# Performance work log

Hardware: AMD Instinct MI355X
Metric: run time of the kernel (lower is better)

## Reference

```python
import jax, jax.numpy as jnp
import numpy as np

H = 50      # hidden_size (fixed in source)
IN = 7      # input_size = len(features)
B = 1024    # batch
T = 512     # seq_len
FC1 = 25
OUT = 1


def setup_inputs() -> dict:
    key = jax.random.key(0)
    ks = jax.random.split(key, 24)
    s = 1.0 / np.sqrt(H)  # PyTorch LSTM/Linear default uniform init scale

    def u(k, shape):
        return jax.random.uniform(k, shape, jnp.float32, -s, s)

    d = {"x": jax.random.normal(ks[0], (B, T, IN), jnp.float32)}
    # 4 stacked LSTM layers total: lstm1 has 2 layers (in=7 then 50), lstm2 has 2 layers (in=50)
    in_sizes = [IN, H, H, H]
    for l, isz in enumerate(in_sizes):
        d[f"Wih{l}"] = u(ks[1 + 4 * l], (4 * H, isz))
        d[f"Whh{l}"] = u(ks[2 + 4 * l], (4 * H, H))
        d[f"bih{l}"] = u(ks[3 + 4 * l], (4 * H,))
        d[f"bhh{l}"] = u(ks[4 + 4 * l], (4 * H,))
    d["W1"] = u(ks[17], (FC1, H))
    d["b1"] = u(ks[18], (FC1,))
    d["W2"] = u(ks[19], (OUT, FC1))
    d["b2"] = u(ks[20], (OUT,))
    return d


def _lstm_layer(x, Wih, Whh, bih, bhh):
    # x: [B, T, in] -> hidden sequence [B, T, H]. PyTorch gate order: i, f, g, o.
    b, t, _ = x.shape
    h = Whh.shape[1]
    # Precompute input projection for all timesteps in one big GEMM: [T, B, 4H]
    xp = jnp.einsum('bti,gi->tbg', x, Wih) + (bih + bhh)

    def step(carry, xt):
        hs, cs = carry
        gates = xt + hs @ Whh.T                      # [B, 4H]
        i, f, g, o = jnp.split(gates, 4, axis=-1)
        i = jax.nn.sigmoid(i)
        f = jax.nn.sigmoid(f)
        g = jnp.tanh(g)
        o = jax.nn.sigmoid(o)
        cs = f * cs + i * g
        hs = o * jnp.tanh(cs)
        return (hs, cs), hs

    h0 = jnp.zeros((b, h), x.dtype)
    _, hseq = jax.lax.scan(step, (h0, h0), xp)       # hseq: [T, B, H]
    return hseq.transpose(1, 0, 2)


def reference(x, Wih0, Whh0, bih0, bhh0, Wih1, Whh1, bih1, bhh1,
              Wih2, Whh2, bih2, bhh2, Wih3, Whh3, bih3, bhh3,
              W1, b1, W2, b2):
    out = x
    layers = [(Wih0, Whh0, bih0, bhh0), (Wih1, Whh1, bih1, bhh1),
              (Wih2, Whh2, bih2, bhh2), (Wih3, Whh3, bih3, bhh3)]
    for Wih, Whh, bih, bhh in layers:
        out = _lstm_layer(out, Wih, Whh, bih, bhh)
    h = out[:, -1, :]                                # last timestep [B, H]
    # dropout is identity in eval mode
    h = jax.nn.relu(h @ W1.T + b1)
    return h @ W2.T + b2                             # [B, 1]
```

## Files before the change

### kernel.cpp

```cpp
#include <hip/hip_runtime.h>


#define H 50
#define INSZ 7
#define TT 512
#define NL 4
#define FC1N 25
#define BPG 4
#define NBLK 256
#define NTHREADS 1024
#define HS 80
#define RROW (BPG * HS)
#define BIASL 56

typedef _Float16 half_t;
typedef __attribute__((ext_vector_type(8))) _Float16 half8_t;
typedef __attribute__((ext_vector_type(4))) float float4_t;

struct Params {
  const float* x;
  const float* Wih[NL];
  const float* Whh[NL];
  const float* bih[NL];
  const float* bhh[NL];
  const float* W1;
  const float* b1;
  const float* W2;
  const float* b2;
  float* out;
};

#define MFMA16(A, B, C) __builtin_amdgcn_mfma_f32_16x16x32_f16((A), (B), (C), 0, 0, 0)
#define EXP2F(x) __builtin_amdgcn_exp2f(x)
#define RCPF(x) __builtin_amdgcn_rcpf(x)

__global__ __launch_bounds__(NTHREADS, 4) void lstm_r7(Params p) {
  __shared__ __align__(16) half_t Xring[64][BPG][HS];
  __shared__ __align__(16) half_t Hbuf[NL - 1][2][BPG][HS];
  __shared__ float fc_h[BPG][H];
  __shared__ float fc1_buf[BPG][FC1N];

  const int tid = threadIdx.x;
  const int b0 = blockIdx.x * BPG;
  const int lane = tid & 63;
  const int quad = lane >> 4;
  const int col = lane & 15;
  const int glay = tid >> 8;
  const int wl = (((tid >> 6) & 3) + glay) & 3;

  half8_t afrag[4][4];
#pragma unroll
  for (int t4 = 0; t4 < 4; ++t4) {
#pragma unroll
    for (int g = 0; g < 4; ++g) {
      half8_t v;
#pragma unroll
      for (int j = 0; j < 8; ++j) {
        const int r = wl * 64 + t4 * 16 + col;
        const int u = r >> 2, q = r & 3;
        const int k = g * 32 + quad * 8 + j;
        float wv = 0.0f;
        if (u < H) {
          const int row = q * H + u;
          if (glay == 0) {
            if (k < INSZ) wv = p.Wih[0][row * INSZ + k];
            else if (k == 7) wv = p.bih[0][row] + p.bhh[0][row];
            else if (k >= 8 && k < 8 + H) wv = p.Whh[0][row * H + (k - 8)];
          } else if (glay == 1) {
            if (k == 7) wv = p.bih[1][row] + p.bhh[1][row];
            else if (k >= 8 && k < 8 + H) wv = p.Wih[1][row * H + (k - 8)];
            else if (k >= 64 && k < 64 + H) wv = p.Whh[1][row * H + (k - 64)];
          } else {
            if (k < H) wv = p.Wih[glay][row * H + k];
            else if (k == BIASL) wv = p.bih[glay][row] + p.bhh[glay][row];
            else if (k >= 64 && k < 64 + H) wv = p.Whh[glay][row * H + (k - 64)];
          }
        }
        v[j] = (half_t)wv;
      }
      afrag[t4][g] = v;
    }
  }

  {
    unsigned* xz = (unsigned*)Xring;
    const int nx = 64 * BPG * HS / 2;
    for (int i = tid; i < nx; i += NTHREADS) xz[i] = 0u;
    unsigned* hz = (unsigned*)Hbuf;
    const int nh = (NL - 1) * 2 * BPG * HS / 2;
    for (int i = tid; i < nh; i += NTHREADS) hz[i] = 0u;
  }
  __syncthreads();
  for (int i = tid; i < 64 * BPG; i += NTHREADS)
    Xring[i >> 2][i & 3][7] = (half_t)1.0f;
  if (tid < (NL - 1) * 2 * BPG) {
    const int l = tid >> 3, pr = (tid >> 2) & 1, b = tid & 3;
    Hbuf[l][pr][b][BIASL] = (half_t)1.0f;
  }
  for (int i = tid; i < 64 * BPG * INSZ; i += NTHREADS) {
    const int t = i / (BPG * INSZ), rem = i % (BPG * INSZ);
    const int b = rem / INSZ, k = rem % INSZ;
    Xring[t][b][k] = (half_t)p.x[((size_t)(b0 + b) * TT + t) * INSZ + k];
  }
  __syncthreads();

  const int bb = col & 3;
  const int tsel = col >> 2;
  const int uu = 16 * wl + 4 * tsel + quad;
  const bool updact = (uu < H);

  const half_t* ring_rd0 = &Xring[0][bb][quad * 8];
  half_t* ring_st0 = &Xring[0][bb][8 + uu];

  const half_t* inb[2] = {nullptr, nullptr};
  const half_t* ownb[2] = {nullptr, nullptr};
  half_t* stb[2] = {nullptr, nullptr};
  if (glay >= 1) {
    ownb[0] = &Hbuf[glay - 1][0][bb][quad * 8];
    ownb[1] = &Hbuf[glay - 1][1][bb][quad * 8];
    stb[0] = &Hbuf[glay - 1][1][bb][uu];
    stb[1] = &Hbuf[glay - 1][0][bb][uu];
  }
  if (glay >= 2) {
    inb[0] = &Hbuf[glay - 2][1][bb][quad * 8];
    inb[1] = &Hbuf[glay - 2][0][bb][quad * 8];
  }
  const int pe = glay & 1, po = pe ^ 1;
  const half_t* in_e = inb[pe];
  const half_t* in_o = inb[po];
  const half_t* own_e = ownb[pe];
  const half_t* own_o = ownb[po];
  half_t* st_e = stb[pe];
  half_t* st_o = stb[po];

  const bool xwave = (glay == 0) && (wl == 3);
  const int rb = lane >> 5;
  const int rt = lane & 31;

  float cst = 0.0f;
  const float4_t fzc = {0.0f, 0.0f, 0.0f, 0.0f};

#define TICK_BODY(PIN, POWN, PST, FCW)                                          \
  {                                                                             \
    float4_t a0 = fzc, a1 = fzc, a2 = fzc, a3 = fzc;                            \
    if (glay == 0) {                                                            \
      const half8_t v0 = *(const half8_t*)(PIN);                                \
      const half8_t v1 = *(const half8_t*)((PIN) + 32);                         \
      if (wl != 3) {                                                            \
        a0 = MFMA16(afrag[0][0], v0, a0); a1 = MFMA16(afrag[1][0], v0, a1);     \
        a2 = MFMA16(afrag[2][0], v0, a2); a3 = MFMA16(afrag[3][0], v0, a3);     \
        a0 = MFMA16(afrag[0][1], v1, a0); a1 = MFMA16(afrag[1][1], v1, a1);     \
        a2 = MFMA16(afrag[2][1], v1, a2); a3 = MFMA16(afrag[3][1], v1, a3);     \
      } else {                                                                  \
        a0 = MFMA16(afrag[0][0], v0, a0);                                       \
        a0 = MFMA16(afrag[0][1], v1, a0);                                       \
      }                                                                         \
    } else {                                                                    \
      const half8_t v0 = *(const half8_t*)(PIN);                                \
      const half8_t v1 = *(const half8_t*)((PIN) + 32);                         \
      const half8_t v2 = *(const half8_t*)(POWN);                               \
      const half8_t v3 = *(const half8_t*)((POWN) + 32);                        \
      if (wl != 3) {                                                            \
        a0 = MFMA16(afrag[0][0], v0, a0); a1 = MFMA16(afrag[1][0], v0, a1);     \
        a2 = MFMA16(afrag[2][0], v0, a2); a3 = MFMA16(afrag[3][0], v0, a3);     \
        a0 = MFMA16(afrag[0][1], v1, a0); a1 = MFMA16(afrag[1][1], v1, a1);     \
        a2 = MFMA16(afrag[2][1], v1, a2); a3 = MFMA16(afrag[3][1], v1, a3);     \
        a0 = MFMA16(afrag[0][2], v2, a0); a1 = MFMA16(afrag[1][2], v2, a1);     \
        a2 = MFMA16(afrag[2][2], v2, a2); a3 = MFMA16(afrag[3][2], v2, a3);     \
        a0 = MFMA16(afrag[0][3], v3, a0); a1 = MFMA16(afrag[1][3], v3, a1);     \
        a2 = MFMA16(afrag[2][3], v3, a2); a3 = MFMA16(afrag[3][3], v3, a3);     \
      } else {                                                                  \
        a0 = MFMA16(afrag[0][0], v0, a0);                                       \
        a0 = MFMA16(afrag[0][1], v1, a0);                                       \
        a0 = MFMA16(afrag[0][2], v2, a0);                                       \
        a0 = MFMA16(afrag[0][3], v3, a0);                                       \
      }                                                                         \
    }                                                                           \
    if (updact) {                                                               \
      const float4_t g01 = (col & 4) ? a1 : a0;                                 \
      const float4_t g23 = (col & 4) ? a3 : a2;                                 \
      const float4_t ga = (col & 8) ? g23 : g01;                                \
      const float di = 1.0f + EXP2F(-1.442695041f * ga[0]);                     \
      const float df = 1.0f + EXP2F(-1.442695041f * ga[1]);                     \
      const float dg = 1.0f + EXP2F(-2.885390082f * ga[2]);                     \
      const float dq = 1.0f + EXP2F(-1.442695041f * ga[3]);                     \
      const float r1 = RCPF(di * df);                                           \
      const float r2 = RCPF(dg * dq);                                           \
      const float gi = r1 * df;                                                 \
      const float gf = r1 * di;                                                 \
      const float gg = 2.0f * (r2 * dq) - 1.0f;                                 \
      const float go = r2 * dg;                                                 \
      cst = gf * cst + gi * gg;                                                 \
      const float dc = 1.0f + EXP2F(-2.885390082f * cst);                       \
      const float h = go * (2.0f * RCPF(dc) - 1.0f);                            \
      *(PST) = (half_t)h;                                                       \
      if (FCW) fc_h[bb][uu] = h;                                                \
    }                                                                           \
  }

  for (int s = 0; s < 3; ++s) {
    const int t = s - glay;
    if (t >= 0) {
      const half_t* rd = ring_rd0 + (s & 63) * RROW;
      half_t* rst = ring_st0 + ((s + 1) & 63) * RROW;
      const int par = t & 1;
      const half_t* pin = (glay <= 1) ? rd : inb[par];
      const half_t* pown = (glay >= 1) ? ownb[par] : rd;
      half_t* pst = (glay == 0) ? rst : stb[par];
      TICK_BODY(pin, pown, pst, false)
    }
    __syncthreads();
  }

  for (int s = 3; s < 511; s += 2) {
    {
      const half_t* rd = ring_rd0 + (s & 63) * RROW;
      half_t* rst = ring_st0 + ((s + 1) & 63) * RROW;
      const half_t* pin = (glay <= 1) ? rd : in_o;
      const half_t* pown = (glay >= 1) ? own_o : rd;
      half_t* pst = (glay == 0) ? rst : st_o;
      TICK_BODY(pin, pown, pst, false)
    }
    __syncthreads();
    {
      const int s2 = s + 1;
      if (xwave && (s2 & 31) == 8 && s2 < 480) {
        const int tb = (s2 & ~31) + 32;
#pragma unroll
        for (int pp = 0; pp < 2; ++pp) {
          const int b = rb + 2 * pp;
          const int t = tb + rt;
          const float* src = &p.x[((size_t)(b0 + b) * TT + t) * INSZ];
          half_t* dst = &Xring[t & 63][b][0];
#pragma unroll
          for (int k = 0; k < INSZ; ++k) dst[k] = (half_t)src[k];
        }
      }
      const half_t* rd = ring_rd0 + (s2 & 63) * RROW;
      half_t* rst = ring_st0 + ((s2 + 1) & 63) * RROW;
      const half_t* pin = (glay <= 1) ? rd : in_e;
      const half_t* pown = (glay >= 1) ? own_e : rd;
      half_t* pst = (glay == 0) ? rst : st_e;
      TICK_BODY(pin, pown, pst, false)
    }
    __syncthreads();
  }

  for (int s = 511; s < TT + NL - 1; ++s) {
    const int t = s - glay;
    if (t < TT) {
      const half_t* rd = ring_rd0 + (s & 63) * RROW;
      half_t* rst = ring_st0 + ((s + 1) & 63) * RROW;
      const int par = t & 1;
      const half_t* pin = (glay <= 1) ? rd : inb[par];
      const half_t* pown = (glay >= 1) ? ownb[par] : rd;
      half_t* pst = (glay == 0) ? rst : stb[par];
      const bool fcw = (glay == NL - 1) && (t == TT - 1);
      TICK_BODY(pin, pown, pst, fcw)
    }
    __syncthreads();
  }

  if (tid < BPG * FC1N) {
    const int b = tid / FC1N, j = tid % FC1N;
    const float* w = p.W1 + j * H;
    float a = p.b1[j];
#pragma unroll
    for (int k = 0; k < H; ++k) a += fc_h[b][k] * w[k];
    fc1_buf[b][j] = fmaxf(a, 0.0f);
  }
  __syncthreads();
  if (tid < BPG) {
    float a = p.b2[0];
#pragma unroll
    for (int j = 0; j < FC1N; ++j) a += fc1_buf[tid][j] * p.W2[j];
    p.out[b0 + tid] = a;
  }
}

extern "C" void kernel_launch(void* const* d_in, const int* in_sizes, int n_in,
                              void* d_out, int out_size, void* d_ws, size_t ws_size,
                              hipStream_t stream) {
  Params p;
  p.x = (const float*)d_in[0];
  for (int l = 0; l < NL; ++l) {
    p.Wih[l] = (const float*)d_in[1 + 4 * l];
    p.Whh[l] = (const float*)d_in[2 + 4 * l];
    p.bih[l] = (const float*)d_in[3 + 4 * l];
    p.bhh[l] = (const float*)d_in[4 + 4 * l];
  }
  p.W1 = (const float*)d_in[17];
  p.b1 = (const float*)d_in[18];
  p.W2 = (const float*)d_in[19];
  p.b2 = (const float*)d_in[20];
  p.out = (float*)d_out;

  hipLaunchKernelGGL(lstm_r7, dim3(NBLK), dim3(NTHREADS), 0, stream, p);
}
```

Baseline: 510.3 us.

## Replace 64-slot LDS ring with double-buffered packed X and compact staging

Swaps the 64-entry ring of full-width rows (x plus layer-0 hidden) for a small staging buffer holding only the 7 input features per step and a double-buffered packed row. One wave copies the next timestep's x into the active packed buffer each tick. Tick addressing becomes fixed per parity, so the per-tick modulo-64 pointer arithmetic goes away, and LDS use drops a lot, which may allow more residency. The cost is an extra LDS copy on every tick inside the critical sync window.

```diff
diff --git a/kernel.cpp b/kernel.cpp
--- a/kernel.cpp
+++ b/kernel.cpp
@@ -10,7 +10,6 @@
 #define NBLK 256
 #define NTHREADS 1024
 #define HS 80
-#define RROW (BPG * HS)
 #define BIASL 56
 
 typedef _Float16 half_t;
@@ -34,9 +33,10 @@
 #define EXP2F(x) __builtin_amdgcn_exp2f(x)
 #define RCPF(x) __builtin_amdgcn_rcpf(x)
 
-__global__ __launch_bounds__(NTHREADS, 4) void lstm_r7(Params p) {
-  __shared__ __align__(16) half_t Xring[64][BPG][HS];
-  __shared__ __align__(16) half_t Hbuf[NL - 1][2][BPG][HS];
+__global__ __launch_bounds__(NTHREADS, 4) void lstm_r8(Params p) {
+  __shared__ __align__(16) half_t Xpack[2][BPG][HS];
+  __shared__ __align__(16) half_t Hbuf[3][2][BPG][HS];
+  __shared__ __align__(16) half_t Xstage[64][BPG][8];
   __shared__ float fc_h[BPG][H];
   __shared__ float fc1_buf[BPG][FC1N];
 
@@ -83,24 +83,24 @@
   }
 
   {
-    unsigned* xz = (unsigned*)Xring;
-    const int nx = 64 * BPG * HS / 2;
-    for (int i = tid; i < nx; i += NTHREADS) xz[i] = 0u;
+    unsigned* xz = (unsigned*)Xpack;
+    for (int i = tid; i < 2 * BPG * HS / 2; i += NTHREADS) xz[i] = 0u;
     unsigned* hz = (unsigned*)Hbuf;
-    const int nh = (NL - 1) * 2 * BPG * HS / 2;
-    for (int i = tid; i < nh; i += NTHREADS) hz[i] = 0u;
+    for (int i = tid; i < 3 * 2 * BPG * HS / 2; i += NTHREADS) hz[i] = 0u;
   }
   __syncthreads();
-  for (int i = tid; i < 64 * BPG; i += NTHREADS)
-    Xring[i >> 2][i & 3][7] = (half_t)1.0f;
-  if (tid < (NL - 1) * 2 * BPG) {
-    const int l = tid >> 3, pr = (tid >> 2) & 1, b = tid & 3;
+  if (tid < 8) {
+    Xpack[tid >> 2][tid & 3][7] = (half_t)1.0f;
+  } else if (tid < 8 + 24) {
+    const int i = tid - 8, l = i >> 3, pr = (i >> 2) & 1, b = i & 3;
     Hbuf[l][pr][b][BIASL] = (half_t)1.0f;
   }
   for (int i = tid; i < 64 * BPG * INSZ; i += NTHREADS) {
     const int t = i / (BPG * INSZ), rem = i % (BPG * INSZ);
     const int b = rem / INSZ, k = rem % INSZ;
-    Xring[t][b][k] = (half_t)p.x[((size_t)(b0 + b) * TT + t) * INSZ + k];
+    const half_t xh = (half_t)p.x[((size_t)(b0 + b) * TT + t) * INSZ + k];
+    Xstage[t][b][k] = xh;
+    if (t == 0) Xpack[0][b][k] = xh;
   }
   __syncthreads();
 
@@ -109,31 +109,41 @@
   const int uu = 16 * wl + 4 * tsel + quad;
   const bool updact = (uu < H);
 
-  const half_t* ring_rd0 = &Xring[0][bb][quad * 8];
-  half_t* ring_st0 = &Xring[0][bb][8 + uu];
-
-  const half_t* inb[2] = {nullptr, nullptr};
-  const half_t* ownb[2] = {nullptr, nullptr};
-  half_t* stb[2] = {nullptr, nullptr};
-  if (glay >= 1) {
-    ownb[0] = &Hbuf[glay - 1][0][bb][quad * 8];
-    ownb[1] = &Hbuf[glay - 1][1][bb][quad * 8];
-    stb[0] = &Hbuf[glay - 1][1][bb][uu];
-    stb[1] = &Hbuf[glay - 1][0][bb][uu];
-  }
-  if (glay >= 2) {
-    inb[0] = &Hbuf[glay - 2][1][bb][quad * 8];
-    inb[1] = &Hbuf[glay - 2][0][bb][quad * 8];
-  }
-  const int pe = glay & 1, po = pe ^ 1;
-  const half_t* in_e = inb[pe];
-  const half_t* in_o = inb[po];
-  const half_t* own_e = ownb[pe];
-  const half_t* own_o = ownb[po];
-  half_t* st_e = stb[pe];
-  half_t* st_o = stb[po];
+  const half_t* pin2[2];
+  const half_t* pown2[2];
+  half_t* pst2[2];
+  if (glay == 0) {
+    pin2[0] = &Xpack[0][bb][quad * 8];
+    pin2[1] = &Xpack[1][bb][quad * 8];
+    pown2[0] = pin2[0];
+    pown2[1] = pin2[1];
+    pst2[0] = &Xpack[1][bb][8 + uu];
+    pst2[1] = &Xpack[0][bb][8 + uu];
+  } else if (glay == 1) {
+    pin2[0] = &Xpack[0][bb][quad * 8];
+    pin2[1] = &Xpack[1][bb][quad * 8];
+    pown2[0] = &Hbuf[0][0][bb][quad * 8];
+    pown2[1] = &Hbuf[0][1][bb][quad * 8];
+    pst2[0] = &Hbuf[0][1][bb][uu];
+    pst2[1] = &Hbuf[0][0][bb][uu];
+  } else {
+    pin2[0] = &Hbuf[glay - 2][0][bb][quad * 8];
+    pin2[1] = &Hbuf[glay - 2][1][bb][quad * 8];
+    pown2[0] = &Hbuf[glay - 1][0][bb][quad * 8];
+    pown2[1] = &Hbuf[glay - 1][1][bb][quad * 8];
+    pst2[0] = &Hbuf[glay - 1][1][bb][uu];
+    pst2[1] = &Hbuf[glay - 1][0][bb][uu];
+  }
+  const half_t* in_e = pin2[0];
+  const half_t* in_o = pin2[1];
+  const half_t* own_e = pown2[0];
+  const half_t* own_o = pown2[1];
+  half_t* st_e = pst2[0];
+  half_t* st_o = pst2[1];
 
   const bool xwave = (glay == 0) && (wl == 3);
+  const bool xcopy = xwave && (lane < BPG * INSZ);
+  const int cb = lane / INSZ, ck = lane % INSZ;
   const int rb = lane >> 5;
   const int rt = lane & 31;
 
@@ -198,28 +208,26 @@
     }                                                                           \
   }
 
+#define XCOPY(S)                                                                \
+  if (xcopy) {                                                                  \
+    const int tn = (S) + 1;                                                     \
+    Xpack[tn & 1][cb][ck] = Xstage[tn & 63][cb][ck];                            \
+  }
+
   for (int s = 0; s < 3; ++s) {
     const int t = s - glay;
     if (t >= 0) {
-      const half_t* rd = ring_rd0 + (s & 63) * RROW;
-      half_t* rst = ring_st0 + ((s + 1) & 63) * RROW;
-      const int par = t & 1;
-      const half_t* pin = (glay <= 1) ? rd : inb[par];
-      const half_t* pown = (glay >= 1) ? ownb[par] : rd;
-      half_t* pst = (glay == 0) ? rst : stb[par];
-      TICK_BODY(pin, pown, pst, false)
-    }
+      const int ph = s & 1;
+      TICK_BODY(pin2[ph], pown2[ph], pst2[ph], false)
+    }
+    XCOPY(s)
     __syncthreads();
   }
 
   for (int s = 3; s < 511; s += 2) {
     {
-      const half_t* rd = ring_rd0 + (s & 63) * RROW;
-      half_t* rst = ring_st0 + ((s + 1) & 63) * RROW;
-      const half_t* pin = (glay <= 1) ? rd : in_o;
-      const half_t* pown = (glay >= 1) ? own_o : rd;
-      half_t* pst = (glay == 0) ? rst : st_o;
-      TICK_BODY(pin, pown, pst, false)
+      TICK_BODY(in_o, own_o, st_o, false)
+      XCOPY(s)
     }
     __syncthreads();
     {
@@ -231,17 +239,13 @@
           const int b = rb + 2 * pp;
           const int t = tb + rt;
           const float* src = &p.x[((size_t)(b0 + b) * TT + t) * INSZ];
-          half_t* dst = &Xring[t & 63][b][0];
+          half_t* dst = &Xstage[t & 63][b][0];
 #pragma unroll
           for (int k = 0; k < INSZ; ++k) dst[k] = (half_t)src[k];
         }
       }
-      const half_t* rd = ring_rd0 + (s2 & 63) * RROW;
-      half_t* rst = ring_st0 + ((s2 + 1) & 63) * RROW;
-      const half_t* pin = (glay <= 1) ? rd : in_e;
-      const half_t* pown = (glay >= 1) ? own_e : rd;
-      half_t* pst = (glay == 0) ? rst : st_e;
-      TICK_BODY(pin, pown, pst, false)
+      TICK_BODY(in_e, own_e, st_e, false)
+      XCOPY(s2)
     }
     __syncthreads();
   }
@@ -249,14 +253,9 @@
   for (int s = 511; s < TT + NL - 1; ++s) {
     const int t = s - glay;
     if (t < TT) {
-      const half_t* rd = ring_rd0 + (s & 63) * RROW;
-      half_t* rst = ring_st0 + ((s + 1) & 63) * RROW;
-      const int par = t & 1;
-      const half_t* pin = (glay <= 1) ? rd : inb[par];
-      const half_t* pown = (glay >= 1) ? ownb[par] : rd;
-      half_t* pst = (glay == 0) ? rst : stb[par];
+      const int ph = s & 1;
       const bool fcw = (glay == NL - 1) && (t == TT - 1);
-      TICK_BODY(pin, pown, pst, fcw)
+      TICK_BODY(pin2[ph], pown2[ph], pst2[ph], fcw)
     }
     __syncthreads();
   }
@@ -295,5 +294,5 @@
   p.b2 = (const float*)d_in[20];
   p.out = (float*)d_out;
 
-  hipLaunchKernelGGL(lstm_r7, dim3(NBLK), dim3(NTHREADS), 0, stream, p);
+  hipLaunchKernelGGL(lstm_r8, dim3(NBLK), dim3(NTHREADS), 0, stream, p);
 }
```

Measured after the change: 474.9 us. 1.07x faster.
